# Performance work log

Measured on AMD Instinct MI355X. Metric: run time of the kernel, lower is better.

The kernel has to match this reference:

```python
import jax, jax.numpy as jnp
import numpy as np

B, T, D, H, HD = 128, 256, 512, 8, 64

def setup_inputs() -> dict:
    key = jax.random.key(0)
    ks = jax.random.split(key, 5)
    scale = 0.02
    return {
        "x": jax.random.normal(ks[0], (B, T, D), dtype=jnp.float32),
        "Wq": jax.random.normal(ks[1], (H, D, HD), dtype=jnp.float32) * scale,
        "Wk": jax.random.normal(ks[2], (H, D, HD), dtype=jnp.float32) * scale,
        "Wv": jax.random.normal(ks[3], (H, D, HD), dtype=jnp.float32) * scale,
        "Wo": jax.random.normal(ks[4], (D, D), dtype=jnp.float32) * scale,
        "bo": jnp.zeros((D,), dtype=jnp.float32),
    }

def reference(x, Wq, Wk, Wv, Wo, bo):
    # Per-head projections, batched over heads: [B,T,D] x [H,D,HD] -> [B,H,T,HD]
    q = jnp.einsum('btd,hdk->bhtk', x, Wq)
    k = jnp.einsum('btd,hdk->bhtk', x, Wk)
    v = jnp.einsum('btd,hdk->bhtk', x, Wv)
    # Scaled scores [B,H,T,T] with causal mask
    scores = jnp.einsum('bhtk,bhsk->bhts', q, k) * (HD ** -0.5)
    causal = jnp.tril(jnp.ones((T, T), dtype=bool))
    scores = jnp.where(causal, scores, jnp.finfo(scores.dtype).min)
    attn = jax.nn.softmax(scores, axis=-1)
    # Dropout is identity at inference.
    out = jnp.einsum('bhts,bhsk->bhtk', attn, v)
    # Concat heads: [B,T,H*HD] == [B,T,D]
    out = out.transpose(0, 2, 1, 3).reshape(B, T, D)
    # Output projection
    return out @ Wo + bo
```

## Files before the change

kernel.cpp:

```cpp
#include <hip/hip_runtime.h>
#include <hip/hip_bf16.h>

typedef __bf16 bf16x8 __attribute__((ext_vector_type(8)));
typedef __bf16 bf16x4 __attribute__((ext_vector_type(4)));
typedef float f32x4 __attribute__((ext_vector_type(4)));
typedef unsigned short u16x8 __attribute__((ext_vector_type(8)));
typedef short s16x4 __attribute__((ext_vector_type(4)));


__device__ __forceinline__ unsigned short f2bf(float f) {
  unsigned u = __float_as_uint(f);
  u += 0x7fffu + ((u >> 16) & 1u);
  return (unsigned short)(u >> 16);
}

__device__ __forceinline__ bf16x4 cvt4(f32x4 v) {
  bf16x4 o;
  o[0] = (__bf16)v[0]; o[1] = (__bf16)v[1]; o[2] = (__bf16)v[2]; o[3] = (__bf16)v[3];
  return o;
}

__device__ __forceinline__ f32x4 mfma16(bf16x4 a, bf16x4 b, f32x4 c) {
#if __has_builtin(__builtin_amdgcn_mfma_f32_16x16x16_bf16)
  return __builtin_amdgcn_mfma_f32_16x16x16_bf16(a, b, c, 0, 0, 0);
#elif __has_builtin(__builtin_amdgcn_mfma_f32_16x16x16bf16_1k)
  return __builtin_amdgcn_mfma_f32_16x16x16bf16_1k(
      __builtin_bit_cast(s16x4, a), __builtin_bit_cast(s16x4, b), c, 0, 0, 0);
#else
  f32x4 d = c;
  asm("v_mfma_f32_16x16x16_bf16 %0, %1, %2, %0" : "+v"(d) : "v"(a), "v"(b));
  return d;
#endif
}

__device__ __forceinline__ void async16(const void* g, void* l) {
  __builtin_amdgcn_global_load_lds(
      (const __attribute__((address_space(1))) void*)g,
      (__attribute__((address_space(3))) void*)l, 16, 0, 0);
}

__global__ __launch_bounds__(256) void k_convert_x(const float* __restrict__ in,
                                                   unsigned short* __restrict__ out) {
  int i = blockIdx.x * 256 + threadIdx.x;
  const float4* p = (const float4*)in + (size_t)i * 2;
  float4 a = p[0], b = p[1];
  u16x8 o;
  o[0] = f2bf(a.x); o[1] = f2bf(a.y); o[2] = f2bf(a.z); o[3] = f2bf(a.w);
  o[4] = f2bf(b.x); o[5] = f2bf(b.y); o[6] = f2bf(b.z); o[7] = f2bf(b.w);
  *((u16x8*)out + i) = o;
}

__global__ __launch_bounds__(256) void k_transpose_w3(const float* __restrict__ w0,
                                                      const float* __restrict__ w1,
                                                      const float* __restrict__ w2,
                                                      unsigned short* __restrict__ out) {
  __shared__ unsigned short tile[64][72];
  int z = blockIdx.z;
  int wsel = z >> 3, hsel = z & 7;
  const float* inb = (wsel == 0 ? w0 : (wsel == 1 ? w1 : w2)) + (size_t)hsel * 512 * 64;
  unsigned short* outb = out + (size_t)z * 512 * 64;
  int r0 = blockIdx.y * 64;
  int tid = threadIdx.x;
  int r = tid >> 2, cq = (tid & 3) * 16;
  const float* src = inb + (size_t)(r0 + r) * 64 + cq;
#pragma unroll
  for (int i = 0; i < 16; i += 4) {
    float4 v = *(const float4*)(src + i);
    tile[r][cq + i + 0] = f2bf(v.x);
    tile[r][cq + i + 1] = f2bf(v.y);
    tile[r][cq + i + 2] = f2bf(v.z);
    tile[r][cq + i + 3] = f2bf(v.w);
  }
  __syncthreads();
  int cr = tid >> 2, rq = (tid & 3) * 16;
  u16x8 o0, o1;
#pragma unroll
  for (int i = 0; i < 8; ++i) o0[i] = tile[rq + i][cr];
#pragma unroll
  for (int i = 0; i < 8; ++i) o1[i] = tile[rq + 8 + i][cr];
  unsigned short* dst = outb + (size_t)cr * 512 + r0 + rq;
  *(u16x8*)dst = o0;
  *(u16x8*)(dst + 8) = o1;
}

__global__ __launch_bounds__(256) void k_transpose_w(const float* __restrict__ in,
                                                     unsigned short* __restrict__ out,
                                                     int rows, int cols) {
  __shared__ unsigned short tile[64][72];
  int c0 = blockIdx.x * 64, r0 = blockIdx.y * 64;
  int tid = threadIdx.x;
  int r = tid >> 2, cq = (tid & 3) * 16;
  const float* src = in + (size_t)(r0 + r) * cols + c0 + cq;
#pragma unroll
  for (int i = 0; i < 16; i += 4) {
    float4 v = *(const float4*)(src + i);
    tile[r][cq + i + 0] = f2bf(v.x);
    tile[r][cq + i + 1] = f2bf(v.y);
    tile[r][cq + i + 2] = f2bf(v.z);
    tile[r][cq + i + 3] = f2bf(v.w);
  }
  __syncthreads();
  int cr = tid >> 2, rq = (tid & 3) * 16;
  u16x8 o0, o1;
#pragma unroll
  for (int i = 0; i < 8; ++i) o0[i] = tile[rq + i][cr];
#pragma unroll
  for (int i = 0; i < 8; ++i) o1[i] = tile[rq + 8 + i][cr];
  unsigned short* dst = out + (size_t)(c0 + cr) * rows + r0 + rq;
  *(u16x8*)dst = o0;
  *(u16x8*)(dst + 8) = o1;
}

template <int KIND>
__global__ __launch_bounds__(512, 1) void k_gemmP(
    const unsigned short* __restrict__ A,
    const unsigned short* __restrict__ Bmat,
    unsigned short* __restrict__ O0,
    unsigned short* __restrict__ O1,
    const float* __restrict__ bo,
    float* __restrict__ outf) {
  __shared__ unsigned short smem[65536];
  const int P = (KIND == 0) ? 64 : 32;
  int xcd = blockIdx.x & 7, g = blockIdx.x >> 3;
  int w = xcd * P + g;
  int mt, nt;
  if (KIND == 0) { mt = w >> 2; nt = w & 3; }
  else           { mt = w >> 1; nt = w & 1; }
  int m0 = mt * 256, n0 = nt * 256;
  int tid = threadIdx.x;
  int wid = tid >> 6, lane = tid & 63;
  int lr = lane & 15, lg = lane >> 4;
  int wm = wid >> 2, wn = wid & 3;

  int srow_off = wid * 16 + (lane >> 3);
  int schunk = (lane & 7) ^ (lane >> 3);
  auto stageA = [&](int kb, int buf, int half) {
#pragma unroll
    for (int j = 0; j < 2; ++j) {
      int row = half * 128 + srow_off + j * 8;
      async16(A + (size_t)(m0 + row) * 512 + kb * 64 + schunk * 8,
              smem + buf * 32768 + half * 8192 + (wid * 2 + j) * 512);
    }
  };
  auto stageB = [&](int kb, int buf, int half) {
#pragma unroll
    for (int j = 0; j < 2; ++j) {
      int row = half * 128 + srow_off + j * 8;
      async16(Bmat + (size_t)(n0 + row) * 512 + kb * 64 + schunk * 8,
              smem + buf * 32768 + 16384 + half * 8192 + (wid * 2 + j) * 512);
    }
  };
  auto lda = [&](int buf, int mi, int k32) -> bf16x8 {
    int row = mi * 32 + wm * 16 + lr;
    int ch = (k32 * 4 + lg) ^ (lr & 7);
    return *(const bf16x8*)&smem[buf * 32768 + row * 64 + ch * 8];
  };
  auto ldb = [&](int buf, int ni, int k32) -> bf16x8 {
    int row = ni * 64 + wn * 16 + lr;
    int ch = (k32 * 4 + lg) ^ (lr & 7);
    return *(const bf16x8*)&smem[buf * 32768 + 16384 + row * 64 + ch * 8];
  };

  f32x4 acc[8][4];
#pragma unroll
  for (int mi = 0; mi < 8; ++mi)
#pragma unroll
    for (int ni = 0; ni < 4; ++ni) acc[mi][ni] = (f32x4){0.f, 0.f, 0.f, 0.f};

#define MF(dst, afrag, bfrag)                                                        \
  if constexpr (KIND == 2)                                                           \
    dst = __builtin_amdgcn_mfma_f32_16x16x32_bf16(afrag, bfrag, dst, 0, 0, 0);       \
  else                                                                               \
    dst = __builtin_amdgcn_mfma_f32_16x16x32_bf16(bfrag, afrag, dst, 0, 0, 0);

  stageA(0, 0, 0); stageB(0, 0, 0); stageA(0, 0, 1); stageB(0, 0, 1);
  asm volatile("s_waitcnt vmcnt(4)" ::: "memory");
  __builtin_amdgcn_s_barrier();
  asm volatile("" ::: "memory");

  bf16x8 a03[4][2], a47[4][2], b01[2][2], b23[2][2];
#pragma unroll
  for (int t = 0; t < 8; ++t) {
    int buf = t & 1, nbuf = buf ^ 1;
    const bool st = (t < 7);
#pragma unroll
    for (int mi = 0; mi < 4; ++mi) { a03[mi][0] = lda(buf, mi, 0); a03[mi][1] = lda(buf, mi, 1); }
#pragma unroll
    for (int ni = 0; ni < 2; ++ni) { b01[ni][0] = ldb(buf, ni, 0); b01[ni][1] = ldb(buf, ni, 1); }
    if (st) stageA(t + 1, nbuf, 0);
    asm volatile("" ::: "memory");
    __builtin_amdgcn_s_setprio(1);
#pragma unroll
    for (int mi = 0; mi < 4; ++mi)
#pragma unroll
      for (int ni = 0; ni < 2; ++ni)
#pragma unroll
        for (int k = 0; k < 2; ++k) { MF(acc[mi][ni], a03[mi][k], b01[ni][k]); }
    __builtin_amdgcn_s_setprio(0);
    if (st) asm volatile("s_waitcnt vmcnt(4)" ::: "memory");
    else    asm volatile("s_waitcnt vmcnt(2)" ::: "memory");
    __builtin_amdgcn_s_barrier();
    asm volatile("" ::: "memory");
#pragma unroll
    for (int mi = 0; mi < 4; ++mi) { a47[mi][0] = lda(buf, mi + 4, 0); a47[mi][1] = lda(buf, mi + 4, 1); }
    if (st) stageB(t + 1, nbuf, 0);
    asm volatile("" ::: "memory");
    __builtin_amdgcn_s_setprio(1);
#pragma unroll
    for (int mi = 0; mi < 4; ++mi)
#pragma unroll
      for (int ni = 0; ni < 2; ++ni)
#pragma unroll
        for (int k = 0; k < 2; ++k) { MF(acc[mi + 4][ni], a47[mi][k], b01[ni][k]); }
    __builtin_amdgcn_s_setprio(0);
    if (st) asm volatile("s_waitcnt vmcnt(4)" ::: "memory");
    else    asm volatile("s_waitcnt vmcnt(0)" ::: "memory");
    __builtin_amdgcn_s_barrier();
    asm volatile("" ::: "memory");
#pragma unroll
    for (int ni = 0; ni < 2; ++ni) { b23[ni][0] = ldb(buf, ni + 2, 0); b23[ni][1] = ldb(buf, ni + 2, 1); }
    if (st) stageA(t + 1, nbuf, 1);
    asm volatile("" ::: "memory");
    __builtin_amdgcn_s_setprio(1);
#pragma unroll
    for (int mi = 0; mi < 4; ++mi)
#pragma unroll
      for (int ni = 0; ni < 2; ++ni)
#pragma unroll
        for (int k = 0; k < 2; ++k) { MF(acc[mi + 4][ni + 2], a47[mi][k], b23[ni][k]); }
    __builtin_amdgcn_s_setprio(0);
    __builtin_amdgcn_s_barrier();
    asm volatile("" ::: "memory");
    if (st) stageB(t + 1, nbuf, 1);
    asm volatile("" ::: "memory");
    __builtin_amdgcn_s_setprio(1);
#pragma unroll
    for (int mi = 0; mi < 4; ++mi)
#pragma unroll
      for (int ni = 0; ni < 2; ++ni)
#pragma unroll
        for (int k = 0; k < 2; ++k) { MF(acc[mi][ni + 2], a03[mi][k], b23[ni][k]); }
    __builtin_amdgcn_s_setprio(0);
    if (st) asm volatile("s_waitcnt vmcnt(4)" ::: "memory");
    __builtin_amdgcn_s_barrier();
    asm volatile("" ::: "memory");
  }
#undef MF

  if constexpr (KIND == 0) {
    int z = n0 >> 9;
    if (z == 0) {
#pragma unroll
      for (int mi = 0; mi < 8; ++mi)
#pragma unroll
        for (int ni = 0; ni < 4; ++ni) acc[mi][ni] *= 0.18033688011112042f;
    }
    int hbase = (n0 & 511) >> 6;
    int hd0 = wn * 16 + lg * 4;
#pragma unroll
    for (int ni = 0; ni < 4; ++ni) {
      unsigned short* outp = (z ? O1 : O0) + (size_t)(mt * 8 + hbase + ni) * 16384;
#pragma unroll
      for (int mi = 0; mi < 8; ++mi) {
        int tq = mi * 32 + wm * 16 + lr;
        *(bf16x4*)&outp[(size_t)tq * 64 + hd0] = cvt4(acc[mi][ni]);
      }
    }
  } else if constexpr (KIND == 1) {
#pragma unroll
    for (int ni = 0; ni < 4; ++ni) {
      int nb = n0 + ni * 64 + wn * 16 + lg * 4;
      float4 b4 = *(const float4*)&bo[nb];
#pragma unroll
      for (int mi = 0; mi < 8; ++mi) {
        int mg = m0 + mi * 32 + wm * 16 + lr;
        float4 o;
        o.x = acc[mi][ni][0] + b4.x; o.y = acc[mi][ni][1] + b4.y;
        o.z = acc[mi][ni][2] + b4.z; o.w = acc[mi][ni][3] + b4.w;
        *(float4*)&outf[(size_t)mg * 512 + nb] = o;
      }
    }
  } else {
    int hbase = n0 >> 6;
    int hd = wn * 16 + lr;
#pragma unroll
    for (int ni = 0; ni < 4; ++ni) {
      unsigned short* outp = O0 + (size_t)(mt * 8 + hbase + ni) * 16384;
#pragma unroll
      for (int mi = 0; mi < 8; ++mi) {
        int tq = mi * 32 + wm * 16 + lg * 4;
        *(bf16x4*)&outp[(size_t)hd * 256 + tq] = cvt4(acc[mi][ni]);
      }
    }
  }
}

__global__ __launch_bounds__(512, 4) void k_attn2(
    const unsigned short* __restrict__ Qb,
    const unsigned short* __restrict__ Kb,
    const unsigned short* __restrict__ Vtb,
    unsigned short* __restrict__ Ob) {
  __shared__ unsigned short Ksh[256 * 72];
  __shared__ unsigned short Vsh[64 * 260];
  int bh = blockIdx.x;
  int tid = threadIdx.x, wid = tid >> 6, lane = tid & 63, lr = lane & 15, lg = lane >> 4;
  int bb = bh >> 3, h = bh & 7;
  const unsigned short* Kg = Kb + (size_t)bh * 16384;
  const unsigned short* Vg = Vtb + (size_t)bh * 16384;
  int4 gk[4], gv[4];
#pragma unroll
  for (int j = 0; j < 4; ++j) {
    int c = tid + j * 512;
    gk[j] = *(const int4*)(Kg + c * 8);
    gv[j] = *(const int4*)(Vg + c * 8);
  }
  int ci0 = wid, ci1 = 15 - wid;
  const unsigned short* q0 = Qb + (size_t)bh * 16384 + (size_t)(ci0 * 16 + lr) * 64 + lg * 8;
  const unsigned short* q1 = Qb + (size_t)bh * 16384 + (size_t)(ci1 * 16 + lr) * 64 + lg * 8;
  bf16x8 bq0a = *(const bf16x8*)q0;
  bf16x8 bq0b = *(const bf16x8*)(q0 + 32);
  bf16x8 bq1a = *(const bf16x8*)q1;
  bf16x8 bq1b = *(const bf16x8*)(q1 + 32);
#pragma unroll
  for (int j = 0; j < 4; ++j) {
    int c = tid + j * 512;
    *(int4*)&Ksh[(c >> 3) * 72 + (c & 7) * 8] = gk[j];
    *(int4*)&Vsh[(c >> 5) * 260 + (c & 31) * 8] = gv[j];
  }
  __syncthreads();

  auto do_chunk = [&](int ci, bf16x8 bqa, bf16x8 bqb) {
    int t0 = ci * 16, trow = t0 + lr;
    int ntV = ci + 1;
    f32x4 acc[16];
#pragma unroll
    for (int nt = 0; nt < 16; ++nt)
      if (nt < ntV) {
        acc[nt] = (f32x4){0.f, 0.f, 0.f, 0.f};
        bf16x8 ak0 = *(const bf16x8*)&Ksh[(nt * 16 + lr) * 72 + lg * 8];
        acc[nt] = __builtin_amdgcn_mfma_f32_16x16x32_bf16(ak0, bqa, acc[nt], 0, 0, 0);
        bf16x8 ak1 = *(const bf16x8*)&Ksh[(nt * 16 + lr) * 72 + 32 + lg * 8];
        acc[nt] = __builtin_amdgcn_mfma_f32_16x16x32_bf16(ak1, bqb, acc[nt], 0, 0, 0);
      }
    float m0c = -3.0e38f, m1c = -3.0e38f;
#pragma unroll
    for (int nt = 0; nt < 16; ++nt)
      if (nt < ntV) {
        if (nt == ci) {
#pragma unroll
          for (int r = 0; r < 4; ++r) {
            float v = acc[nt][r];
            if (lg * 4 + r > lr) v = -1.0e30f;
            acc[nt][r] = v;
          }
        }
        m0c = fmaxf(m0c, fmaxf(acc[nt][0], acc[nt][1]));
        m1c = fmaxf(m1c, fmaxf(acc[nt][2], acc[nt][3]));
      }
    float m = fmaxf(m0c, m1c);
    m = fmaxf(m, __shfl_xor(m, 16));
    m = fmaxf(m, __shfl_xor(m, 32));
    float s4[4] = {0.f, 0.f, 0.f, 0.f};
    bf16x4 pk[16];
#pragma unroll
    for (int nt = 0; nt < 16; ++nt)
      if (nt < ntV) {
#pragma unroll
        for (int r = 0; r < 4; ++r) {
          float p = exp2f(acc[nt][r] - m);
          s4[r] += p;
          pk[nt][r] = (__bf16)p;
        }
      }
    float s = (s4[0] + s4[1]) + (s4[2] + s4[3]);
    s += __shfl_xor(s, 16);
    s += __shfl_xor(s, 32);
    float inv = 1.0f / s;
    f32x4 aco[4];
#pragma unroll
    for (int vt = 0; vt < 4; ++vt) aco[vt] = (f32x4){0.f, 0.f, 0.f, 0.f};
#pragma unroll
    for (int nt = 0; nt < 16; ++nt)
      if (nt < ntV) {
#pragma unroll
        for (int vt = 0; vt < 4; ++vt) {
          bf16x4 av = *(const bf16x4*)&Vsh[(vt * 16 + lr) * 260 + nt * 16 + lg * 4];
          aco[vt] = mfma16(av, pk[nt], aco[vt]);
        }
      }
    unsigned short* obase = Ob + (size_t)(bb * 256 + trow) * 512 + h * 64 + lg * 4;
#pragma unroll
    for (int vt = 0; vt < 4; ++vt) {
      bf16x4 ov;
#pragma unroll
      for (int r = 0; r < 4; ++r) ov[r] = (__bf16)(aco[vt][r] * inv);
      *(bf16x4*)(obase + vt * 16) = ov;
    }
  };

  do_chunk(ci0, bq0a, bq0b);
  do_chunk(ci1, bq1a, bq1b);
}

extern "C" void kernel_launch(void* const* d_in, const int* in_sizes, int n_in,
                              void* d_out, int out_size, void* d_ws, size_t ws_size,
                              hipStream_t stream) {
  (void)in_sizes; (void)n_in; (void)out_size; (void)ws_size;
  const float* x = (const float*)d_in[0];
  const float* Wq = (const float*)d_in[1];
  const float* Wk = (const float*)d_in[2];
  const float* Wv = (const float*)d_in[3];
  const float* Wo = (const float*)d_in[4];
  const float* bo = (const float*)d_in[5];
  float* out = (float*)d_out;
  char* ws = (char*)d_ws;
  const size_t MB = 1024 * 1024;
  unsigned short* Qb = (unsigned short*)(ws);
  unsigned short* Kb = (unsigned short*)(ws + 32 * MB);
  unsigned short* Vtb = (unsigned short*)(ws + 64 * MB);
  unsigned short* xb = (unsigned short*)(ws + 96 * MB);
  unsigned short* Wqt = (unsigned short*)(ws + 128 * MB);
  unsigned short* Wkt = Wqt + 262144;
  unsigned short* Wvt = Wkt + 262144;
  unsigned short* Wot = Wvt + 262144;

  hipLaunchKernelGGL(k_convert_x, dim3(8192), dim3(256), 0, stream, x, xb);
  hipLaunchKernelGGL(k_transpose_w3, dim3(1, 8, 24), dim3(256), 0, stream, Wq, Wk, Wv, Wqt);
  hipLaunchKernelGGL(k_transpose_w, dim3(8, 8, 1), dim3(256), 0, stream, Wo, Wot, 512, 512);
  hipLaunchKernelGGL((k_gemmP<0>), dim3(512), dim3(512), 0, stream,
                     xb, Wqt, Qb, Kb, (const float*)nullptr, (float*)nullptr);
  hipLaunchKernelGGL((k_gemmP<2>), dim3(256), dim3(512), 0, stream,
                     xb, Wvt, Vtb, (unsigned short*)nullptr, (const float*)nullptr, (float*)nullptr);
  hipLaunchKernelGGL(k_attn2, dim3(1024), dim3(512), 0, stream, Qb, Kb, Vtb, xb);
  hipLaunchKernelGGL((k_gemmP<1>), dim3(256), dim3(512), 0, stream,
                     xb, Wot, (unsigned short*)nullptr, (unsigned short*)nullptr, bo, out);
}
```

Measured before the change: 157.9 us.

## Fuse QKV projections into one GEMM launch with smaller tiles and triple buffering

Merges the Q/K and V projection GEMMs into a single kernel over a concatenated weight, and merges the two weight-transpose kernels into one launch. The GEMM tile shrinks from 256x256 with a K-step of 64 to 128x256 with a K-step of 32. The staging moves from double to triple buffering with fewer barriers per step, and the smaller shared-memory footprint allows up to four blocks per CU. This cuts launch count and tail effects and should raise occupancy and latency hiding, at the cost of less data reuse per tile and more global loads per FLOP.

```diff
diff --git a/kernel.cpp b/kernel.cpp
--- a/kernel.cpp
+++ b/kernel.cpp
@@ -50,19 +50,29 @@
   *((u16x8*)out + i) = o;
 }
 
-__global__ __launch_bounds__(256) void k_transpose_w3(const float* __restrict__ w0,
-                                                      const float* __restrict__ w1,
-                                                      const float* __restrict__ w2,
-                                                      unsigned short* __restrict__ out) {
+__global__ __launch_bounds__(256) void k_transpose_all(const float* __restrict__ Wq,
+                                                       const float* __restrict__ Wk,
+                                                       const float* __restrict__ Wv,
+                                                       const float* __restrict__ Wo,
+                                                       unsigned short* __restrict__ Wqkv,
+                                                       unsigned short* __restrict__ Wot) {
   __shared__ unsigned short tile[64][72];
   int z = blockIdx.z;
-  int wsel = z >> 3, hsel = z & 7;
-  const float* inb = (wsel == 0 ? w0 : (wsel == 1 ? w1 : w2)) + (size_t)hsel * 512 * 64;
-  unsigned short* outb = out + (size_t)z * 512 * 64;
+  const float* inb;
+  unsigned short* outb;
+  int incols, c0;
+  if (z < 3) {
+    const float* w = (z == 0) ? Wq : (z == 1 ? Wk : Wv);
+    inb = w + (size_t)blockIdx.x * 512 * 64;
+    outb = Wqkv + ((size_t)z * 8 + blockIdx.x) * 32768;
+    incols = 64; c0 = 0;
+  } else {
+    inb = Wo; outb = Wot; incols = 512; c0 = blockIdx.x * 64;
+  }
   int r0 = blockIdx.y * 64;
   int tid = threadIdx.x;
   int r = tid >> 2, cq = (tid & 3) * 16;
-  const float* src = inb + (size_t)(r0 + r) * 64 + cq;
+  const float* src = inb + (size_t)(r0 + r) * incols + c0 + cq;
 #pragma unroll
   for (int i = 0; i < 16; i += 4) {
     float4 v = *(const float4*)(src + i);
@@ -78,202 +88,105 @@
   for (int i = 0; i < 8; ++i) o0[i] = tile[rq + i][cr];
 #pragma unroll
   for (int i = 0; i < 8; ++i) o1[i] = tile[rq + 8 + i][cr];
-  unsigned short* dst = outb + (size_t)cr * 512 + r0 + rq;
+  unsigned short* dst = outb + (size_t)(c0 + cr) * 512 + r0 + rq;
   *(u16x8*)dst = o0;
   *(u16x8*)(dst + 8) = o1;
 }
 
-__global__ __launch_bounds__(256) void k_transpose_w(const float* __restrict__ in,
-                                                     unsigned short* __restrict__ out,
-                                                     int rows, int cols) {
-  __shared__ unsigned short tile[64][72];
-  int c0 = blockIdx.x * 64, r0 = blockIdx.y * 64;
-  int tid = threadIdx.x;
-  int r = tid >> 2, cq = (tid & 3) * 16;
-  const float* src = in + (size_t)(r0 + r) * cols + c0 + cq;
-#pragma unroll
-  for (int i = 0; i < 16; i += 4) {
-    float4 v = *(const float4*)(src + i);
-    tile[r][cq + i + 0] = f2bf(v.x);
-    tile[r][cq + i + 1] = f2bf(v.y);
-    tile[r][cq + i + 2] = f2bf(v.z);
-    tile[r][cq + i + 3] = f2bf(v.w);
-  }
-  __syncthreads();
-  int cr = tid >> 2, rq = (tid & 3) * 16;
-  u16x8 o0, o1;
-#pragma unroll
-  for (int i = 0; i < 8; ++i) o0[i] = tile[rq + i][cr];
-#pragma unroll
-  for (int i = 0; i < 8; ++i) o1[i] = tile[rq + 8 + i][cr];
-  unsigned short* dst = out + (size_t)(c0 + cr) * rows + r0 + rq;
-  *(u16x8*)dst = o0;
-  *(u16x8*)(dst + 8) = o1;
-}
-
-template <int KIND>
-__global__ __launch_bounds__(512, 1) void k_gemmP(
-    const unsigned short* __restrict__ A,
-    const unsigned short* __restrict__ Bmat,
-    unsigned short* __restrict__ O0,
-    unsigned short* __restrict__ O1,
-    const float* __restrict__ bo,
-    float* __restrict__ outf) {
-  __shared__ unsigned short smem[65536];
-  const int P = (KIND == 0) ? 64 : 32;
-  int xcd = blockIdx.x & 7, g = blockIdx.x >> 3;
-  int w = xcd * P + g;
-  int mt, nt;
-  if (KIND == 0) { mt = w >> 2; nt = w & 3; }
-  else           { mt = w >> 1; nt = w & 1; }
-  int m0 = mt * 256, n0 = nt * 256;
-  int tid = threadIdx.x;
-  int wid = tid >> 6, lane = tid & 63;
-  int lr = lane & 15, lg = lane >> 4;
+template <bool SWAP, int EPI>
+__device__ __forceinline__ void gemm_body(
+    unsigned short* smem,
+    const unsigned short* __restrict__ A, const unsigned short* __restrict__ Bm,
+    unsigned short* __restrict__ O0, unsigned short* __restrict__ O1,
+    const float* __restrict__ bo, float* __restrict__ outf,
+    int m0, int n0, int mt, bool qscale) {
+  int tid = threadIdx.x, wid = tid >> 6, lane = tid & 63, lr = lane & 15, lg = lane >> 4;
   int wm = wid >> 2, wn = wid & 3;
-
-  int srow_off = wid * 16 + (lane >> 3);
-  int schunk = (lane & 7) ^ (lane >> 3);
-  auto stageA = [&](int kb, int buf, int half) {
-#pragma unroll
-    for (int j = 0; j < 2; ++j) {
-      int row = half * 128 + srow_off + j * 8;
-      async16(A + (size_t)(m0 + row) * 512 + kb * 64 + schunk * 8,
-              smem + buf * 32768 + half * 8192 + (wid * 2 + j) * 512);
-    }
-  };
-  auto stageB = [&](int kb, int buf, int half) {
-#pragma unroll
-    for (int j = 0; j < 2; ++j) {
-      int row = half * 128 + srow_off + j * 8;
-      async16(Bmat + (size_t)(n0 + row) * 512 + kb * 64 + schunk * 8,
-              smem + buf * 32768 + 16384 + half * 8192 + (wid * 2 + j) * 512);
-    }
-  };
-  auto lda = [&](int buf, int mi, int k32) -> bf16x8 {
-    int row = mi * 32 + wm * 16 + lr;
-    int ch = (k32 * 4 + lg) ^ (lr & 7);
-    return *(const bf16x8*)&smem[buf * 32768 + row * 64 + ch * 8];
-  };
-  auto ldb = [&](int buf, int ni, int k32) -> bf16x8 {
-    int row = ni * 64 + wn * 16 + lr;
-    int ch = (k32 * 4 + lg) ^ (lr & 7);
-    return *(const bf16x8*)&smem[buf * 32768 + 16384 + row * 64 + ch * 8];
-  };
-
-  f32x4 acc[8][4];
-#pragma unroll
-  for (int mi = 0; mi < 8; ++mi)
+  int arow = tid >> 2;
+  int sk8 = (tid & 3) ^ ((tid >> 3) & 3);
+  const unsigned short* asrc = A + (size_t)(m0 + arow) * 512 + sk8 * 8;
+  const unsigned short* bsrc0 = Bm + (size_t)(n0 + arow) * 512 + sk8 * 8;
+  const unsigned short* bsrc1 = Bm + (size_t)(n0 + 128 + arow) * 512 + sk8 * 8;
+  int rdsw = (lg ^ ((lr >> 1) & 3)) * 8;
+
+  f32x4 acc[4][4];
+#pragma unroll
+  for (int mi = 0; mi < 4; ++mi)
 #pragma unroll
     for (int ni = 0; ni < 4; ++ni) acc[mi][ni] = (f32x4){0.f, 0.f, 0.f, 0.f};
 
-#define MF(dst, afrag, bfrag)                                                        \
-  if constexpr (KIND == 2)                                                           \
-    dst = __builtin_amdgcn_mfma_f32_16x16x32_bf16(afrag, bfrag, dst, 0, 0, 0);       \
-  else                                                                               \
-    dst = __builtin_amdgcn_mfma_f32_16x16x32_bf16(bfrag, afrag, dst, 0, 0, 0);
-
-  stageA(0, 0, 0); stageB(0, 0, 0); stageA(0, 0, 1); stageB(0, 0, 1);
-  asm volatile("s_waitcnt vmcnt(4)" ::: "memory");
+#define STAGE(kb, buf)                                                   \
+  {                                                                      \
+    unsigned short* base_ = smem + (buf) * 12288;                        \
+    async16(asrc + (kb) * 32, base_ + wid * 512);                        \
+    async16(bsrc0 + (kb) * 32, base_ + 4096 + wid * 512);                \
+    async16(bsrc1 + (kb) * 32, base_ + 8192 + wid * 512);                \
+  }
+
+  STAGE(0, 0)
+  STAGE(1, 1)
+  asm volatile("s_waitcnt vmcnt(3)" ::: "memory");
   __builtin_amdgcn_s_barrier();
   asm volatile("" ::: "memory");
 
-  bf16x8 a03[4][2], a47[4][2], b01[2][2], b23[2][2];
-#pragma unroll
-  for (int t = 0; t < 8; ++t) {
-    int buf = t & 1, nbuf = buf ^ 1;
-    const bool st = (t < 7);
-#pragma unroll
-    for (int mi = 0; mi < 4; ++mi) { a03[mi][0] = lda(buf, mi, 0); a03[mi][1] = lda(buf, mi, 1); }
-#pragma unroll
-    for (int ni = 0; ni < 2; ++ni) { b01[ni][0] = ldb(buf, ni, 0); b01[ni][1] = ldb(buf, ni, 1); }
-    if (st) stageA(t + 1, nbuf, 0);
+#pragma unroll
+  for (int t = 0; t < 16; ++t) {
+    int buf = t % 3;
+    bf16x8 a[4], b[4];
+#pragma unroll
+    for (int mi = 0; mi < 4; ++mi)
+      a[mi] = *(const bf16x8*)&smem[buf * 12288 + (wm * 64 + mi * 16 + lr) * 32 + rdsw];
+#pragma unroll
+    for (int ni = 0; ni < 4; ++ni)
+      b[ni] = *(const bf16x8*)&smem[buf * 12288 + 4096 + (wn * 64 + ni * 16 + lr) * 32 + rdsw];
+    if (t < 14) STAGE(t + 2, (t + 2) % 3)
     asm volatile("" ::: "memory");
     __builtin_amdgcn_s_setprio(1);
 #pragma unroll
     for (int mi = 0; mi < 4; ++mi)
 #pragma unroll
-      for (int ni = 0; ni < 2; ++ni)
-#pragma unroll
-        for (int k = 0; k < 2; ++k) { MF(acc[mi][ni], a03[mi][k], b01[ni][k]); }
+      for (int ni = 0; ni < 4; ++ni) {
+        if (SWAP)
+          acc[mi][ni] = __builtin_amdgcn_mfma_f32_16x16x32_bf16(b[ni], a[mi], acc[mi][ni], 0, 0, 0);
+        else
+          acc[mi][ni] = __builtin_amdgcn_mfma_f32_16x16x32_bf16(a[mi], b[ni], acc[mi][ni], 0, 0, 0);
+      }
     __builtin_amdgcn_s_setprio(0);
-    if (st) asm volatile("s_waitcnt vmcnt(4)" ::: "memory");
-    else    asm volatile("s_waitcnt vmcnt(2)" ::: "memory");
+    if (t < 14)       asm volatile("s_waitcnt vmcnt(3)" ::: "memory");
+    else if (t == 14) asm volatile("s_waitcnt vmcnt(0)" ::: "memory");
     __builtin_amdgcn_s_barrier();
     asm volatile("" ::: "memory");
-#pragma unroll
-    for (int mi = 0; mi < 4; ++mi) { a47[mi][0] = lda(buf, mi + 4, 0); a47[mi][1] = lda(buf, mi + 4, 1); }
-    if (st) stageB(t + 1, nbuf, 0);
-    asm volatile("" ::: "memory");
-    __builtin_amdgcn_s_setprio(1);
-#pragma unroll
-    for (int mi = 0; mi < 4; ++mi)
-#pragma unroll
-      for (int ni = 0; ni < 2; ++ni)
-#pragma unroll
-        for (int k = 0; k < 2; ++k) { MF(acc[mi + 4][ni], a47[mi][k], b01[ni][k]); }
-    __builtin_amdgcn_s_setprio(0);
-    if (st) asm volatile("s_waitcnt vmcnt(4)" ::: "memory");
-    else    asm volatile("s_waitcnt vmcnt(0)" ::: "memory");
-    __builtin_amdgcn_s_barrier();
-    asm volatile("" ::: "memory");
-#pragma unroll
-    for (int ni = 0; ni < 2; ++ni) { b23[ni][0] = ldb(buf, ni + 2, 0); b23[ni][1] = ldb(buf, ni + 2, 1); }
-    if (st) stageA(t + 1, nbuf, 1);
-    asm volatile("" ::: "memory");
-    __builtin_amdgcn_s_setprio(1);
-#pragma unroll
-    for (int mi = 0; mi < 4; ++mi)
-#pragma unroll
-      for (int ni = 0; ni < 2; ++ni)
-#pragma unroll
-        for (int k = 0; k < 2; ++k) { MF(acc[mi + 4][ni + 2], a47[mi][k], b23[ni][k]); }
-    __builtin_amdgcn_s_setprio(0);
-    __builtin_amdgcn_s_barrier();
-    asm volatile("" ::: "memory");
-    if (st) stageB(t + 1, nbuf, 1);
-    asm volatile("" ::: "memory");
-    __builtin_amdgcn_s_setprio(1);
-#pragma unroll
-    for (int mi = 0; mi < 4; ++mi)
-#pragma unroll
-      for (int ni = 0; ni < 2; ++ni)
-#pragma unroll
-        for (int k = 0; k < 2; ++k) { MF(acc[mi][ni + 2], a03[mi][k], b23[ni][k]); }
-    __builtin_amdgcn_s_setprio(0);
-    if (st) asm volatile("s_waitcnt vmcnt(4)" ::: "memory");
-    __builtin_amdgcn_s_barrier();
-    asm volatile("" ::: "memory");
-  }
-#undef MF
-
-  if constexpr (KIND == 0) {
+  }
+#undef STAGE
+
+  int bb = mt >> 1, t0 = (mt & 1) * 128;
+  if constexpr (EPI == 0) {
+    if (qscale) {
+#pragma unroll
+      for (int mi = 0; mi < 4; ++mi)
+#pragma unroll
+        for (int ni = 0; ni < 4; ++ni) acc[mi][ni] *= 0.18033688011112042f;
+    }
     int z = n0 >> 9;
-    if (z == 0) {
-#pragma unroll
-      for (int mi = 0; mi < 8; ++mi)
-#pragma unroll
-        for (int ni = 0; ni < 4; ++ni) acc[mi][ni] *= 0.18033688011112042f;
-    }
-    int hbase = (n0 & 511) >> 6;
-    int hd0 = wn * 16 + lg * 4;
+    int h = ((n0 & 511) >> 6) + wn;
+    unsigned short* outp = (z ? O1 : O0) + (size_t)(bb * 8 + h) * 16384;
 #pragma unroll
     for (int ni = 0; ni < 4; ++ni) {
-      unsigned short* outp = (z ? O1 : O0) + (size_t)(mt * 8 + hbase + ni) * 16384;
-#pragma unroll
-      for (int mi = 0; mi < 8; ++mi) {
-        int tq = mi * 32 + wm * 16 + lr;
+      int hd0 = ni * 16 + lg * 4;
+#pragma unroll
+      for (int mi = 0; mi < 4; ++mi) {
+        int tq = t0 + wm * 64 + mi * 16 + lr;
         *(bf16x4*)&outp[(size_t)tq * 64 + hd0] = cvt4(acc[mi][ni]);
       }
     }
-  } else if constexpr (KIND == 1) {
+  } else if constexpr (EPI == 1) {
 #pragma unroll
     for (int ni = 0; ni < 4; ++ni) {
-      int nb = n0 + ni * 64 + wn * 16 + lg * 4;
+      int nb = n0 + wn * 64 + ni * 16 + lg * 4;
       float4 b4 = *(const float4*)&bo[nb];
 #pragma unroll
-      for (int mi = 0; mi < 8; ++mi) {
-        int mg = m0 + mi * 32 + wm * 16 + lr;
+      for (int mi = 0; mi < 4; ++mi) {
+        int mg = m0 + wm * 64 + mi * 16 + lr;
         float4 o;
         o.x = acc[mi][ni][0] + b4.x; o.y = acc[mi][ni][1] + b4.y;
         o.z = acc[mi][ni][2] + b4.z; o.w = acc[mi][ni][3] + b4.w;
@@ -281,18 +194,47 @@
       }
     }
   } else {
-    int hbase = n0 >> 6;
-    int hd = wn * 16 + lr;
+    int h = ((n0 & 511) >> 6) + wn;
+    unsigned short* outp = O0 + (size_t)(bb * 8 + h) * 16384;
 #pragma unroll
     for (int ni = 0; ni < 4; ++ni) {
-      unsigned short* outp = O0 + (size_t)(mt * 8 + hbase + ni) * 16384;
-#pragma unroll
-      for (int mi = 0; mi < 8; ++mi) {
-        int tq = mi * 32 + wm * 16 + lg * 4;
+      int hd = ni * 16 + lr;
+#pragma unroll
+      for (int mi = 0; mi < 4; ++mi) {
+        int tq = t0 + wm * 64 + mi * 16 + lg * 4;
         *(bf16x4*)&outp[(size_t)hd * 256 + tq] = cvt4(acc[mi][ni]);
       }
     }
   }
+}
+
+__global__ __launch_bounds__(512, 4) void k_qkv3(
+    const unsigned short* __restrict__ xb,
+    const unsigned short* __restrict__ Wt,
+    unsigned short* __restrict__ Qb,
+    unsigned short* __restrict__ Kb,
+    unsigned short* __restrict__ Vtb) {
+  __shared__ unsigned short smem[36864];
+  int xcd = blockIdx.x & 7, g = blockIdx.x >> 3;
+  int w = xcd * 192 + g;
+  int mt = w / 6, nt = w % 6;
+  int m0 = mt * 128, n0 = nt * 256;
+  if ((n0 >> 9) < 2)
+    gemm_body<true, 0>(smem, xb, Wt, Qb, Kb, nullptr, nullptr, m0, n0, mt, n0 < 512);
+  else
+    gemm_body<false, 2>(smem, xb, Wt, Vtb, nullptr, nullptr, nullptr, m0, n0, mt, false);
+}
+
+__global__ __launch_bounds__(512, 4) void k_oproj(
+    const unsigned short* __restrict__ Ab,
+    const unsigned short* __restrict__ Wot,
+    const float* __restrict__ bo,
+    float* __restrict__ outf) {
+  __shared__ unsigned short smem[36864];
+  int xcd = blockIdx.x & 7, g = blockIdx.x >> 3;
+  int w = xcd * 64 + g;
+  int mt = w >> 1, nt = w & 1;
+  gemm_body<true, 1>(smem, Ab, Wot, nullptr, nullptr, bo, outf, mt * 128, nt * 256, mt, false);
 }
 
 __global__ __launch_bounds__(512, 4) void k_attn2(
@@ -419,19 +361,13 @@
   unsigned short* Kb = (unsigned short*)(ws + 32 * MB);
   unsigned short* Vtb = (unsigned short*)(ws + 64 * MB);
   unsigned short* xb = (unsigned short*)(ws + 96 * MB);
-  unsigned short* Wqt = (unsigned short*)(ws + 128 * MB);
-  unsigned short* Wkt = Wqt + 262144;
-  unsigned short* Wvt = Wkt + 262144;
-  unsigned short* Wot = Wvt + 262144;
+  unsigned short* Wqkv = (unsigned short*)(ws + 128 * MB);
+  unsigned short* Wot = Wqkv + 786432;
 
   hipLaunchKernelGGL(k_convert_x, dim3(8192), dim3(256), 0, stream, x, xb);
-  hipLaunchKernelGGL(k_transpose_w3, dim3(1, 8, 24), dim3(256), 0, stream, Wq, Wk, Wv, Wqt);
-  hipLaunchKernelGGL(k_transpose_w, dim3(8, 8, 1), dim3(256), 0, stream, Wo, Wot, 512, 512);
-  hipLaunchKernelGGL((k_gemmP<0>), dim3(512), dim3(512), 0, stream,
-                     xb, Wqt, Qb, Kb, (const float*)nullptr, (float*)nullptr);
-  hipLaunchKernelGGL((k_gemmP<2>), dim3(256), dim3(512), 0, stream,
-                     xb, Wvt, Vtb, (unsigned short*)nullptr, (const float*)nullptr, (float*)nullptr);
+  hipLaunchKernelGGL(k_transpose_all, dim3(8, 8, 4), dim3(256), 0, stream,
+                     Wq, Wk, Wv, Wo, Wqkv, Wot);
+  hipLaunchKernelGGL(k_qkv3, dim3(1536), dim3(512), 0, stream, xb, Wqkv, Qb, Kb, Vtb);
   hipLaunchKernelGGL(k_attn2, dim3(1024), dim3(512), 0, stream, Qb, Kb, Vtb, xb);
-  hipLaunchKernelGGL((k_gemmP<1>), dim3(256), dim3(512), 0, stream,
-                     xb, Wot, (unsigned short*)nullptr, (unsigned short*)nullptr, bo, out);
-}
+  hipLaunchKernelGGL(k_oproj, dim3(512), dim3(512), 0, stream, xb, Wot, bo, out);
+}
```

Result: slower. 161.3 us (+2.1%).
